# Kernel tuning notes

Hardware: AMD Instinct MI355X
Metric: run time of the kernel (lower is better)

Reference implementation:

```python
import jax, jax.numpy as jnp
import numpy as np
import math

N_ATOMS = 10000
N_EDGES = 100000
NF = 32          # num_radial_features
NK = 32          # radial basis size
CUTOFF = 5.0
L_BOND = 2       # max_basis_degree
L_IN = 2         # degree of atomic descriptors
L_OUT = 4        # max_degree of tensor product output
EPS = 1e-6

# ---------- real Clebsch-Gordan coefficients (built once in numpy) ----------

def _fact(n):
    return math.factorial(n)

def _cg_complex(j1, m1, j2, m2, j3, m3):
    if m1 + m2 != m3 or not (abs(j1 - j2) <= j3 <= j1 + j2):
        return 0.0
    if abs(m1) > j1 or abs(m2) > j2 or abs(m3) > j3:
        return 0.0
    pref = math.sqrt((2 * j3 + 1) * _fact(j3 + j1 - j2) * _fact(j3 - j1 + j2)
                     * _fact(j1 + j2 - j3) / _fact(j1 + j2 + j3 + 1))
    pref *= math.sqrt(_fact(j3 + m3) * _fact(j3 - m3) * _fact(j1 - m1)
                      * _fact(j1 + m1) * _fact(j2 - m2) * _fact(j2 + m2))
    s = 0.0
    for k in range(0, j1 + j2 - j3 + 1):
        d = [k, j1 + j2 - j3 - k, j1 - m1 - k, j2 + m2 - k, j3 - j2 + m1 + k, j3 - j1 - m2 + k]
        if min(d) < 0:
            continue
        s += (-1) ** k / float(_fact(d[0]) * _fact(d[1]) * _fact(d[2]) * _fact(d[3]) * _fact(d[4]) * _fact(d[5]))
    return pref * s

def _U(l):
    # unitary complex->real spherical harmonic change of basis, m ordered -l..l
    U = np.zeros((2 * l + 1, 2 * l + 1), dtype=complex)
    for m in range(-l, l + 1):
        i = m + l
        if m > 0:
            U[i, m + l] = (-1) ** m / math.sqrt(2.0)
            U[i, -m + l] = 1.0 / math.sqrt(2.0)
        elif m == 0:
            U[i, l] = 1.0
        else:
            U[i, m + l] = 1j / math.sqrt(2.0)
            U[i, -m + l] = -1j * (-1) ** (-m) / math.sqrt(2.0)
    return U

def _real_cg(l1, l2, l3):
    base = np.zeros((2 * l1 + 1, 2 * l2 + 1, 2 * l3 + 1))
    for m1 in range(-l1, l1 + 1):
        for m2 in range(-l2, l2 + 1):
            m3 = m1 + m2
            if abs(m3) <= l3:
                base[m1 + l1, m2 + l2, m3 + l3] = _cg_complex(l1, m1, l2, m2, l3, m3)
    C = np.einsum('ax,by,cz,xyz->abc', _U(l1).conj(), _U(l2).conj(), _U(l3), base)
    C = C.real if (l1 + l2 + l3) % 2 == 0 else C.imag  # odd paths -> pseudotensor channel
    return C.astype(np.float32)

def _build_paths():
    paths = []
    for l1 in range(L_BOND + 1):
        for l2 in range(L_IN + 1):
            for l3 in range(abs(l1 - l2), min(l1 + l2, L_OUT) + 1):
                par = (l1 + l2 + l3) % 2
                paths.append((l1, l2, l3, par, jnp.asarray(_real_cg(l1, l2, l3))))
    return paths

PATHS = _build_paths()
N_PATHS = len(PATHS)  # 19 paths

# ---------- equivariant building blocks ----------

def _dense(x, W, b):
    y = jnp.einsum('epmf,fg->epmg', x, W)
    return y.at[..., 0, :].add(b)

def _layernorm(x, gamma, beta):
    # equivariant LayerNorm: standard LN on scalars, per-degree RMS norm on l>0 blocks
    s = x[..., 0:1, :]
    mu = jnp.mean(s, axis=-1, keepdims=True)
    var = jnp.var(s, axis=-1, keepdims=True)
    parts = [(s - mu) / jnp.sqrt(var + EPS) * gamma[0] + beta]
    for l in range(1, L_IN + 1):
        blk = x[..., l * l:(l + 1) ** 2, :]
        rms = jnp.sqrt(jnp.mean(blk * blk, axis=(-2, -1), keepdims=True) + EPS)
        parts.append(blk / rms * gamma[l])
    return jnp.concatenate(parts, axis=-2)

def _mish_gate(x):
    s = x[..., 0:1, :]
    sp = jax.nn.softplus(s)
    t = jnp.tanh(sp)
    act = s * t
    d = t + s * (1.0 - t * t) * jax.nn.sigmoid(s)
    return jnp.concatenate([act, x[..., 1:, :] * d], axis=-2)

def _sph(u):
    # real spherical harmonics up to l=2, Racah normalization, m order -l..l
    x, y, z = u[:, 0], u[:, 1], u[:, 2]
    s3 = math.sqrt(3.0)
    return jnp.stack([jnp.ones_like(x), y, z, x,
                      s3 * x * y, s3 * y * z, 0.5 * (3.0 * z * z - 1.0),
                      s3 * x * z, 0.5 * s3 * (x * x - y * y)], axis=-1)  # (E, 9)

def _bond_basis(disp):
    r = jnp.sqrt(jnp.sum(disp * disp, axis=-1))          # (E,)
    u = disp / jnp.maximum(r, 1e-12)[:, None]
    centers = jnp.linspace(0.0, CUTOFF, NK)
    gamma = 0.5 * (NK / CUTOFF) ** 2
    rad = jnp.exp(-gamma * (r[:, None] - centers[None, :]) ** 2)  # (E, NK)
    cut = jnp.where(r < CUTOFF, 0.5 * (jnp.cos(jnp.pi * r / CUTOFF) + 1.0), 0.0)
    rad = rad * cut[:, None]
    sh = _sph(u)                                          # (E, 9)
    return sh[:, None, :, None] * rad[:, None, None, :]   # (E, 1, 9, NK)

def _tensor_product(x1, x2, tp_w):
    # CG-sparse equivariant tensor product with per-path per-feature weights
    E = x1.shape[0]
    F = x1.shape[-1]
    out = jnp.zeros((E, 2, (L_OUT + 1) ** 2, F), dtype=x1.dtype)
    for pidx, (l1, l2, l3, par, C) in enumerate(PATHS):
        a = x1[:, 0, l1 * l1:(l1 + 1) ** 2, :]
        b = x2[:, 0, l2 * l2:(l2 + 1) ** 2, :]
        seg = jnp.einsum('abc,eaf,ebf->ecf', C, a, b) * tp_w[pidx][None, None, :]
        out = out.at[:, par, l3 * l3:(l3 + 1) ** 2, :].add(seg)
    return out

# ---------- harness ----------

def setup_inputs() -> dict:
    key = jax.random.key(0)
    ks = jax.random.split(key, 8)
    atomic_descriptors = jax.random.normal(ks[0], (N_ATOMS, 1, (L_IN + 1) ** 2, NF), dtype=jnp.float32)
    neighbour_indices = jax.random.randint(ks[1], (N_EDGES, 2), 0, N_ATOMS, dtype=jnp.int32)
    neighbour_displacements = jax.random.normal(ks[2], (N_EDGES, 3), dtype=jnp.float32)
    W1 = jax.random.normal(ks[3], (NF, NF), dtype=jnp.float32) / math.sqrt(NF)
    b1 = jnp.zeros((NF,), dtype=jnp.float32)
    ln_gamma = jnp.ones((L_IN + 1, NF), dtype=jnp.float32)
    ln_beta = jnp.zeros((NF,), dtype=jnp.float32)
    W2 = jax.random.normal(ks[4], (NF, NF), dtype=jnp.float32) / math.sqrt(NF)
    b2 = jnp.zeros((NF,), dtype=jnp.float32)
    Wb = jax.random.normal(ks[5], (NK, NF), dtype=jnp.float32) / math.sqrt(NK)
    bb = jnp.zeros((NF,), dtype=jnp.float32)
    tp_w = jax.random.normal(ks[6], (N_PATHS, NF), dtype=jnp.float32) / math.sqrt(N_PATHS)
    return {"atomic_descriptors": atomic_descriptors,
            "neighbour_indices": neighbour_indices,
            "neighbour_displacements": neighbour_displacements,
            "W1": W1, "b1": b1, "ln_gamma": ln_gamma, "ln_beta": ln_beta,
            "W2": W2, "b2": b2, "Wb": Wb, "bb": bb, "tp_w": tp_w}

def reference(atomic_descriptors, neighbour_indices, neighbour_displacements,
              W1, b1, ln_gamma, ln_beta, W2, b2, Wb, bb, tp_w):
    i, j = neighbour_indices[:, 0], neighbour_indices[:, 1]
    y = atomic_descriptors[i] + atomic_descriptors[j]         # (E, 1, 9, F) gather + add
    y0 = _dense(y, W1, b1)
    y = _layernorm(y0, ln_gamma, ln_beta)
    y = _mish_gate(y)
    y = _dense(y, W2, b2) + y0                                # residual MLP
    basis = _bond_basis(neighbour_displacements)              # (E, 1, 9, NK)
    bexp = _dense(basis, Wb, bb)                              # (E, 1, 9, F)
    return _tensor_product(bexp, y, tp_w)                     # (E, 2, 25, F)
```

## Files before the change

kernel.cpp:

```cpp
#include <hip/hip_runtime.h>
#include <utility>

namespace cg {

constexpr double FACT[13] = {1.,1.,2.,6.,24.,120.,720.,5040.,40320.,362880.,
                             3628800.,39916800.,479001600.};

constexpr double csqrt(double x){
  if (x <= 0.0) return 0.0;
  double g = x > 1.0 ? x : 1.0;
  for (int i = 0; i < 80; i++) g = 0.5*(g + x/g);
  return g;
}

constexpr double cg_complex(int j1,int m1,int j2,int m2,int j3,int m3){
  if (m1+m2 != m3) return 0.0;
  int dj = j1>j2 ? j1-j2 : j2-j1;
  if (j3 < dj || j3 > j1+j2) return 0.0;
  int am1 = m1<0?-m1:m1, am2 = m2<0?-m2:m2, am3 = m3<0?-m3:m3;
  if (am1>j1 || am2>j2 || am3>j3) return 0.0;
  double pref = csqrt((2.0*j3+1.0)*FACT[j3+j1-j2]*FACT[j3-j1+j2]*FACT[j1+j2-j3]
                      /FACT[j1+j2+j3+1]);
  pref *= csqrt(FACT[j3+m3]*FACT[j3-m3]*FACT[j1-m1]*FACT[j1+m1]
               *FACT[j2-m2]*FACT[j2+m2]);
  double s = 0.0;
  for (int k = 0; k <= j1+j2-j3; k++){
    int d1=j1+j2-j3-k, d2=j1-m1-k, d3=j2+m2-k, d4=j3-j2+m1+k, d5=j3-j1-m2+k;
    if (d1<0||d2<0||d3<0||d4<0||d5<0) continue;
    double den = FACT[k]*FACT[d1]*FACT[d2]*FACT[d3]*FACT[d4]*FACT[d5];
    s += ((k&1) ? -1.0 : 1.0)/den;
  }
  return pref*s;
}

struct CD { double re, im; };
struct UMat { CD m[9][9]; };

constexpr UMat makeU(int l){
  UMat U{};
  const double is2 = 1.0/csqrt(2.0);
  for (int mm = -l; mm <= l; mm++){
    int i = mm + l;
    if (mm > 0){
      U.m[i][ mm+l] = CD{((mm&1)?-1.0:1.0)*is2, 0.0};
      U.m[i][-mm+l] = CD{is2, 0.0};
    } else if (mm == 0){
      U.m[i][l] = CD{1.0, 0.0};
    } else {
      int nm = -mm;
      U.m[i][mm+l] = CD{0.0, is2};
      U.m[i][nm+l] = CD{0.0, -((nm&1)?-1.0:1.0)*is2};
    }
  }
  return U;
}

struct CGT { double c[5][5][9]; };

constexpr CGT realCG(int l1,int l2,int l3){
  double base[5][5][9] = {};
  for (int m1 = -l1; m1 <= l1; m1++)
    for (int m2 = -l2; m2 <= l2; m2++){
      int m3 = m1 + m2;
      if (m3 >= -l3 && m3 <= l3)
        base[m1+l1][m2+l2][m3+l3] = cg_complex(l1,m1,l2,m2,l3,m3);
    }
  UMat U1 = makeU(l1), U2 = makeU(l2), U3 = makeU(l3);
  CGT R{};
  const int n1 = 2*l1+1, n2 = 2*l2+1, n3 = 2*l3+1;
  const bool even = ((l1+l2+l3)&1) == 0;
  for (int a = 0; a < n1; a++)
    for (int b = 0; b < n2; b++)
      for (int c = 0; c < n3; c++){
        double sre = 0.0, sim = 0.0;
        for (int x = 0; x < n1; x++){
          CD u1 = U1.m[a][x];
          if (u1.re == 0.0 && u1.im == 0.0) continue;
          u1.im = -u1.im;
          for (int y = 0; y < n2; y++){
            CD u2 = U2.m[b][y];
            if (u2.re == 0.0 && u2.im == 0.0) continue;
            u2.im = -u2.im;
            CD t12{u1.re*u2.re - u1.im*u2.im, u1.re*u2.im + u1.im*u2.re};
            for (int z = 0; z < n3; z++){
              double bs = base[x][y][z];
              if (bs == 0.0) continue;
              CD u3 = U3.m[c][z];
              if (u3.re == 0.0 && u3.im == 0.0) continue;
              sre += (t12.re*u3.re - t12.im*u3.im)*bs;
              sim += (t12.re*u3.im + t12.im*u3.re)*bs;
            }
          }
        }
        R.c[a][b][c] = even ? sre : sim;
      }
  return R;
}

constexpr int MAXE = 805;
struct Table {
  int n, np;
  int oc[MAXE]; int ia[MAXE]; int ib[MAXE]; int ip[MAXE];
  float v[MAXE];
};

constexpr Table buildTable(){
  Table t{};
  int n = 0, p = 0;
  for (int l1 = 0; l1 <= 2; l1++)
    for (int l2 = 0; l2 <= 2; l2++){
      int lo = l1 > l2 ? l1-l2 : l2-l1;
      int hi = (l1+l2) < 4 ? (l1+l2) : 4;
      for (int l3 = lo; l3 <= hi; l3++){
        int par = (l1+l2+l3)&1;
        CGT C = realCG(l1,l2,l3);
        for (int a = 0; a < 2*l1+1; a++)
          for (int b = 0; b < 2*l2+1; b++)
            for (int c = 0; c < 2*l3+1; c++){
              double v = C.c[a][b][c];
              if (v > 1e-10 || v < -1e-10){
                t.oc[n] = par*25 + l3*l3 + c;
                t.ia[n] = l1*l1 + a;
                t.ib[n] = l2*l2 + b;
                t.ip[n] = p;
                t.v[n]  = (float)v;
                n++;
              }
            }
        p++;
      }
    }
  t.n = n; t.np = p;
  return t;
}

constexpr Table T = buildTable();
static_assert(T.np == 19, "path count mismatch vs reference PATHS");
static_assert(T.n >= 19 && T.n <= MAXE, "nnz sanity");

}

template <int... Es>
__device__ __forceinline__ void tp_accum(float (&acc)[50], const float (&bx)[9],
                                         const float (&y2)[9], const float (&wv)[19],
                                         std::integer_sequence<int, Es...>){
  ( (acc[cg::T.oc[Es]] +=
       (cg::T.v[Es] * bx[cg::T.ia[Es]]) * (y2[cg::T.ib[Es]] * wv[cg::T.ip[Es]])), ... );
}

__global__ __launch_bounds__(256) void btmd_kernel(
    const float* __restrict__ A,  const int* __restrict__ NI,
    const float* __restrict__ D,
    const float* __restrict__ W1, const float* __restrict__ b1,
    const float* __restrict__ GM, const float* __restrict__ BT,
    const float* __restrict__ W2, const float* __restrict__ b2,
    const float* __restrict__ Wb, const float* __restrict__ bb,
    const float* __restrict__ TW, float* __restrict__ out, int nE)
{
  __shared__ alignas(16) float stg[8][288];
  __shared__ alignas(16) float radl[8][32];

  const int lane = threadIdx.x & 31;
  const int grp  = threadIdx.x >> 5;
  const int edge = blockIdx.x * 8 + grp;
  if (edge >= nE) return;

  const int ia_ = NI[2*edge + 0];
  const int ja_ = NI[2*edge + 1];
  const float* Ai = A + (size_t)ia_*288 + lane;
  const float* Aj = A + (size_t)ja_*288 + lane;
#pragma unroll
  for (int m = 0; m < 9; m++)
    stg[grp][m*32 + lane] = Ai[m*32] + Aj[m*32];

  const float dx = D[3*edge+0], dy = D[3*edge+1], dz = D[3*edge+2];
  const float r    = sqrtf(dx*dx + dy*dy + dz*dz);
  const float rinv = 1.0f / fmaxf(r, 1e-12f);
  const float ux = dx*rinv, uy = dy*rinv, uz = dz*rinv;
  const float S3 = 1.7320508075688772f;
  const float sh1 = uy, sh2 = uz, sh3 = ux;
  const float sh4 = S3*ux*uy, sh5 = S3*uy*uz;
  const float sh6 = 0.5f*(3.0f*uz*uz - 1.0f);
  const float sh7 = S3*ux*uz, sh8 = 0.5f*S3*(ux*ux - uy*uy);
  {
    const float ck  = (5.0f/31.0f)*(float)lane;
    const float dr  = r - ck;
    const float cut = (r < 5.0f)
        ? 0.5f*(__cosf(0.6283185307179586f*r) + 1.0f) : 0.0f;
    radl[grp][lane] = __expf(-20.48f*dr*dr) * cut;
  }

  float y0[9];
  {
    float w1c[32];
#pragma unroll
    for (int f = 0; f < 32; f++) w1c[f] = W1[f*32 + lane];
    const float b1v = b1[lane];
#pragma unroll
    for (int m = 0; m < 9; m++){
      float acc = (m == 0) ? b1v : 0.0f;
      const float4* s4 = (const float4*)(&stg[grp][m*32]);
#pragma unroll
      for (int q = 0; q < 8; q++){
        float4 a = s4[q];
        acc += a.x*w1c[4*q+0] + a.y*w1c[4*q+1] + a.z*w1c[4*q+2] + a.w*w1c[4*q+3];
      }
      y0[m] = acc;
    }
  }

  const float s0 = y0[0];
  float sum0 = s0, sumsq0 = s0*s0;
  float ss1 = y0[1]*y0[1] + y0[2]*y0[2] + y0[3]*y0[3];
  float ss2 = y0[4]*y0[4] + y0[5]*y0[5] + y0[6]*y0[6] + y0[7]*y0[7] + y0[8]*y0[8];
#pragma unroll
  for (int off = 16; off >= 1; off >>= 1){
    sum0   += __shfl_xor(sum0,   off, 32);
    sumsq0 += __shfl_xor(sumsq0, off, 32);
    ss1    += __shfl_xor(ss1,    off, 32);
    ss2    += __shfl_xor(ss2,    off, 32);
  }
  const float mu  = sum0*(1.0f/32.0f);
  const float var = sumsq0*(1.0f/32.0f) - mu*mu;
  const float g0 = GM[lane], g1 = GM[32+lane], g2 = GM[64+lane];
  const float shat = (s0 - mu)*rsqrtf(var + 1e-6f)*g0 + BT[lane];
  const float inv1 = rsqrtf(ss1*(1.0f/96.0f)  + 1e-6f)*g1;
  const float inv2 = rsqrtf(ss2*(1.0f/160.0f) + 1e-6f)*g2;

  const float s    = shat;
  const float sp   = fmaxf(s, 0.0f) + log1pf(__expf(-fabsf(s)));
  const float e2   = __expf(2.0f*sp);
  const float t    = 1.0f - 2.0f/(e2 + 1.0f);
  const float sig  = 1.0f/(1.0f + __expf(-s));
  const float dgat = t + s*(1.0f - t*t)*sig;
  const float act  = s*t;

  stg[grp][lane] = act;
#pragma unroll
  for (int m = 1; m < 4; m++) stg[grp][m*32 + lane] = y0[m]*inv1*dgat;
#pragma unroll
  for (int m = 4; m < 9; m++) stg[grp][m*32 + lane] = y0[m]*inv2*dgat;

  float y2[9];
  {
    float w2c[32];
#pragma unroll
    for (int f = 0; f < 32; f++) w2c[f] = W2[f*32 + lane];
    const float b2v = b2[lane];
#pragma unroll
    for (int m = 0; m < 9; m++){
      float acc = (m == 0) ? b2v : 0.0f;
      const float4* s4 = (const float4*)(&stg[grp][m*32]);
#pragma unroll
      for (int q = 0; q < 8; q++){
        float4 a = s4[q];
        acc += a.x*w2c[4*q+0] + a.y*w2c[4*q+1] + a.z*w2c[4*q+2] + a.w*w2c[4*q+3];
      }
      y2[m] = acc + y0[m];
    }
  }

  float gf;
  {
    float wbc[32];
#pragma unroll
    for (int k = 0; k < 32; k++) wbc[k] = Wb[k*32 + lane];
    float acc = 0.0f;
    const float4* r4 = (const float4*)(&radl[grp][0]);
#pragma unroll
    for (int q = 0; q < 8; q++){
      float4 a = r4[q];
      acc += a.x*wbc[4*q+0] + a.y*wbc[4*q+1] + a.z*wbc[4*q+2] + a.w*wbc[4*q+3];
    }
    gf = acc;
  }
  float bx[9];
  bx[0] = gf + bb[lane];
  bx[1] = sh1*gf; bx[2] = sh2*gf; bx[3] = sh3*gf; bx[4] = sh4*gf;
  bx[5] = sh5*gf; bx[6] = sh6*gf; bx[7] = sh7*gf; bx[8] = sh8*gf;

  float wv[19];
#pragma unroll
  for (int p = 0; p < 19; p++) wv[p] = TW[p*32 + lane];
  float acc[50];
#pragma unroll
  for (int c = 0; c < 50; c++) acc[c] = 0.0f;
  tp_accum(acc, bx, y2, wv, std::make_integer_sequence<int, cg::T.n>{});

  float* op = out + (size_t)edge*1600 + lane;
#pragma unroll
  for (int c = 0; c < 50; c++)
    __builtin_nontemporal_store(acc[c], op + c*32);
}

extern "C" void kernel_launch(void* const* d_in, const int* in_sizes, int n_in,
                              void* d_out, int out_size, void* d_ws, size_t ws_size,
                              hipStream_t stream)
{
  const float* A  = (const float*)d_in[0];
  const int*   NI = (const int*)  d_in[1];
  const float* D  = (const float*)d_in[2];
  const float* W1 = (const float*)d_in[3];
  const float* b1 = (const float*)d_in[4];
  const float* GM = (const float*)d_in[5];
  const float* BT = (const float*)d_in[6];
  const float* W2 = (const float*)d_in[7];
  const float* b2 = (const float*)d_in[8];
  const float* Wb = (const float*)d_in[9];
  const float* bb = (const float*)d_in[10];
  const float* TW = (const float*)d_in[11];
  float* out = (float*)d_out;

  const int nE = in_sizes[1] / 2;
  dim3 grid((nE + 7) / 8), block(256);
  btmd_kernel<<<grid, block, 0, stream>>>(A, NI, D, W1, b1, GM, BT, W2, b2,
                                          Wb, bb, TW, out, nE);
}
```

Measured before the change: 702.3 us.

## Persistent grid-stride kernel with prefetched gathers, LDS-staged weights, per-row TP stores

Converts the one-edge-per-warp launch into a persistent grid-stride kernel capped at 1024 blocks. Each block stages transposed W1/W2/Wb in shared memory once and keeps per-lane parameters in registers. The loop software-pipelines the next edge's descriptor gathers and the indices and displacements two edges ahead. The tensor product is reorganized by output channel so each output row is computed and stored immediately instead of holding 50 accumulators, aiming to cut register pressure (launch_bounds 256,4). The risk is extra registers from prefetch buffers and possible LDS bank conflicts on the transposed weight reads.

```diff
diff --git a/kernel.cpp b/kernel.cpp
--- a/kernel.cpp
+++ b/kernel.cpp
@@ -138,17 +138,54 @@
 static_assert(T.np == 19, "path count mismatch vs reference PATHS");
 static_assert(T.n >= 19 && T.n <= MAXE, "nnz sanity");
 
-}
-
-template <int... Es>
-__device__ __forceinline__ void tp_accum(float (&acc)[50], const float (&bx)[9],
-                                         const float (&y2)[9], const float (&wv)[19],
-                                         std::integer_sequence<int, Es...>){
-  ( (acc[cg::T.oc[Es]] +=
-       (cg::T.v[Es] * bx[cg::T.ia[Es]]) * (y2[cg::T.ib[Es]] * wv[cg::T.ip[Es]])), ... );
-}
-
-__global__ __launch_bounds__(256) void btmd_kernel(
+struct Table2 {
+  int off[51];
+  int ia[MAXE]; int ib[MAXE]; int ip[MAXE];
+  float v[MAXE];
+};
+
+constexpr Table2 buildTable2(){
+  Table2 s{};
+  int pos = 0;
+  for (int oc = 0; oc < 50; oc++){
+    s.off[oc] = pos;
+    for (int e = 0; e < T.n; e++){
+      if (T.oc[e] == oc){
+        s.ia[pos] = T.ia[e]; s.ib[pos] = T.ib[e];
+        s.ip[pos] = T.ip[e]; s.v[pos]  = T.v[e];
+        pos++;
+      }
+    }
+  }
+  s.off[50] = pos;
+  return s;
+}
+
+constexpr Table2 T2 = buildTable2();
+static_assert(T2.off[50] == T.n, "resort lost entries");
+
+}
+
+template <int OC, int B, int... Ks>
+__device__ __forceinline__ float tp_row(const float (&bx)[9], const float (&y2)[9],
+                                        const float (&wv)[19],
+                                        std::integer_sequence<int, Ks...>){
+  float a = 0.0f;
+  ((a += (cg::T2.v[B+Ks] * bx[cg::T2.ia[B+Ks]]) * (y2[cg::T2.ib[B+Ks]] * wv[cg::T2.ip[B+Ks]])), ...);
+  return a;
+}
+
+template <int... OCs>
+__device__ __forceinline__ void tp_store_all(const float (&bx)[9], const float (&y2)[9],
+                                             const float (&wv)[19], float* __restrict__ op,
+                                             std::integer_sequence<int, OCs...>){
+  ((__builtin_nontemporal_store(
+       tp_row<OCs, cg::T2.off[OCs]>(bx, y2, wv,
+         std::make_integer_sequence<int, cg::T2.off[OCs+1] - cg::T2.off[OCs]>{}),
+       op + OCs*32)), ...);
+}
+
+__global__ __launch_bounds__(256, 4) void btmd_kernel(
     const float* __restrict__ A,  const int* __restrict__ NI,
     const float* __restrict__ D,
     const float* __restrict__ W1, const float* __restrict__ b1,
@@ -159,138 +196,200 @@
 {
   __shared__ alignas(16) float stg[8][288];
   __shared__ alignas(16) float radl[8][32];
-
-  const int lane = threadIdx.x & 31;
-  const int grp  = threadIdx.x >> 5;
-  const int edge = blockIdx.x * 8 + grp;
-  if (edge >= nE) return;
-
-  const int ia_ = NI[2*edge + 0];
-  const int ja_ = NI[2*edge + 1];
-  const float* Ai = A + (size_t)ia_*288 + lane;
-  const float* Aj = A + (size_t)ja_*288 + lane;
-#pragma unroll
-  for (int m = 0; m < 9; m++)
-    stg[grp][m*32 + lane] = Ai[m*32] + Aj[m*32];
-
-  const float dx = D[3*edge+0], dy = D[3*edge+1], dz = D[3*edge+2];
-  const float r    = sqrtf(dx*dx + dy*dy + dz*dz);
-  const float rinv = 1.0f / fmaxf(r, 1e-12f);
-  const float ux = dx*rinv, uy = dy*rinv, uz = dz*rinv;
-  const float S3 = 1.7320508075688772f;
-  const float sh1 = uy, sh2 = uz, sh3 = ux;
-  const float sh4 = S3*ux*uy, sh5 = S3*uy*uz;
-  const float sh6 = 0.5f*(3.0f*uz*uz - 1.0f);
-  const float sh7 = S3*ux*uz, sh8 = 0.5f*S3*(ux*ux - uy*uy);
+  __shared__ alignas(16) float w1t[32*36];
+  __shared__ alignas(16) float w2t[32*36];
+  __shared__ alignas(16) float wbt[32*36];
+
+  const int tid  = threadIdx.x;
+  const int lane = tid & 31;
+  const int grp  = tid >> 5;
+
   {
-    const float ck  = (5.0f/31.0f)*(float)lane;
-    const float dr  = r - ck;
-    const float cut = (r < 5.0f)
-        ? 0.5f*(__cosf(0.6283185307179586f*r) + 1.0f) : 0.0f;
-    radl[grp][lane] = __expf(-20.48f*dr*dr) * cut;
-  }
-
-  float y0[9];
+    const int idx = tid*4;
+    const int f = idx >> 5, g = idx & 31;
+    const float4 a1 = *(const float4*)(W1 + idx);
+    const float4 a2 = *(const float4*)(W2 + idx);
+    const float4 a3 = *(const float4*)(Wb + idx);
+    w1t[(g+0)*36+f]=a1.x; w1t[(g+1)*36+f]=a1.y; w1t[(g+2)*36+f]=a1.z; w1t[(g+3)*36+f]=a1.w;
+    w2t[(g+0)*36+f]=a2.x; w2t[(g+1)*36+f]=a2.y; w2t[(g+2)*36+f]=a2.z; w2t[(g+3)*36+f]=a2.w;
+    wbt[(g+0)*36+f]=a3.x; wbt[(g+1)*36+f]=a3.y; wbt[(g+2)*36+f]=a3.z; wbt[(g+3)*36+f]=a3.w;
+  }
+
+  float wv[19];
+#pragma unroll
+  for (int p = 0; p < 19; p++) wv[p] = TW[p*32 + lane];
+  const float b1v = b1[lane], b2v = b2[lane], bbv = bb[lane];
+  const float g0 = GM[lane], g1 = GM[32+lane], g2 = GM[64+lane], btv = BT[lane];
+
+  __syncthreads();
+
+  const int stride = gridDim.x * 8;
+  int e = blockIdx.x * 8 + grp;
+  if (e >= nE) return;
+
+  float pa[9], pb[9];
+  float cdx, cdy, cdz;
+  int   i1 = 0, j1 = 0;
+  float d1x = 0.f, d1y = 0.f, d1z = 0.f;
+  int   i2 = 0, j2 = 0;
+  float d2x = 0.f, d2y = 0.f, d2z = 0.f;
+
   {
-    float w1c[32];
-#pragma unroll
-    for (int f = 0; f < 32; f++) w1c[f] = W1[f*32 + lane];
-    const float b1v = b1[lane];
-#pragma unroll
-    for (int m = 0; m < 9; m++){
-      float acc = (m == 0) ? b1v : 0.0f;
-      const float4* s4 = (const float4*)(&stg[grp][m*32]);
+    const int2 nn = *(const int2*)(NI + 2*e);
+    cdx = D[3*e]; cdy = D[3*e+1]; cdz = D[3*e+2];
+    const float* Ai = A + (size_t)nn.x*288 + lane;
+    const float* Aj = A + (size_t)nn.y*288 + lane;
+#pragma unroll
+    for (int m = 0; m < 9; m++){ pa[m] = Ai[m*32]; pb[m] = Aj[m*32]; }
+    const int en1 = e + stride;
+    if (en1 < nE){
+      const int2 n1 = *(const int2*)(NI + 2*en1);
+      i1 = n1.x; j1 = n1.y;
+      d1x = D[3*en1]; d1y = D[3*en1+1]; d1z = D[3*en1+2];
+    }
+  }
+
+  for (; e < nE; e += stride){
+    const int en1 = e + stride;
+    const int en2 = e + 2*stride;
+
+    if (en2 < nE){
+      const int2 n2 = *(const int2*)(NI + 2*en2);
+      i2 = n2.x; j2 = n2.y;
+      d2x = D[3*en2]; d2y = D[3*en2+1]; d2z = D[3*en2+2];
+    }
+
+#pragma unroll
+    for (int m = 0; m < 9; m++) stg[grp][m*32 + lane] = pa[m] + pb[m];
+
+    const float r    = sqrtf(cdx*cdx + cdy*cdy + cdz*cdz);
+    const float rinv = 1.0f / fmaxf(r, 1e-12f);
+    const float ux = cdx*rinv, uy = cdy*rinv, uz = cdz*rinv;
+    {
+      const float ck  = (5.0f/31.0f)*(float)lane;
+      const float dr  = r - ck;
+      const float cut = (r < 5.0f)
+          ? 0.5f*(__cosf(0.6283185307179586f*r) + 1.0f) : 0.0f;
+      radl[grp][lane] = __expf(-20.48f*dr*dr) * cut;
+    }
+
+    if (en1 < nE){
+      const float* Ai = A + (size_t)i1*288 + lane;
+      const float* Aj = A + (size_t)j1*288 + lane;
+#pragma unroll
+      for (int m = 0; m < 9; m++){ pa[m] = Ai[m*32]; pb[m] = Aj[m*32]; }
+    }
+
+    float y0[9];
+    {
+      float w1c[32];
+      const float4* wp = (const float4*)&w1t[lane*36];
 #pragma unroll
       for (int q = 0; q < 8; q++){
-        float4 a = s4[q];
-        acc += a.x*w1c[4*q+0] + a.y*w1c[4*q+1] + a.z*w1c[4*q+2] + a.w*w1c[4*q+3];
-      }
-      y0[m] = acc;
-    }
-  }
-
-  const float s0 = y0[0];
-  float sum0 = s0, sumsq0 = s0*s0;
-  float ss1 = y0[1]*y0[1] + y0[2]*y0[2] + y0[3]*y0[3];
-  float ss2 = y0[4]*y0[4] + y0[5]*y0[5] + y0[6]*y0[6] + y0[7]*y0[7] + y0[8]*y0[8];
-#pragma unroll
-  for (int off = 16; off >= 1; off >>= 1){
-    sum0   += __shfl_xor(sum0,   off, 32);
-    sumsq0 += __shfl_xor(sumsq0, off, 32);
-    ss1    += __shfl_xor(ss1,    off, 32);
-    ss2    += __shfl_xor(ss2,    off, 32);
-  }
-  const float mu  = sum0*(1.0f/32.0f);
-  const float var = sumsq0*(1.0f/32.0f) - mu*mu;
-  const float g0 = GM[lane], g1 = GM[32+lane], g2 = GM[64+lane];
-  const float shat = (s0 - mu)*rsqrtf(var + 1e-6f)*g0 + BT[lane];
-  const float inv1 = rsqrtf(ss1*(1.0f/96.0f)  + 1e-6f)*g1;
-  const float inv2 = rsqrtf(ss2*(1.0f/160.0f) + 1e-6f)*g2;
-
-  const float s    = shat;
-  const float sp   = fmaxf(s, 0.0f) + log1pf(__expf(-fabsf(s)));
-  const float e2   = __expf(2.0f*sp);
-  const float t    = 1.0f - 2.0f/(e2 + 1.0f);
-  const float sig  = 1.0f/(1.0f + __expf(-s));
-  const float dgat = t + s*(1.0f - t*t)*sig;
-  const float act  = s*t;
-
-  stg[grp][lane] = act;
-#pragma unroll
-  for (int m = 1; m < 4; m++) stg[grp][m*32 + lane] = y0[m]*inv1*dgat;
-#pragma unroll
-  for (int m = 4; m < 9; m++) stg[grp][m*32 + lane] = y0[m]*inv2*dgat;
-
-  float y2[9];
-  {
-    float w2c[32];
-#pragma unroll
-    for (int f = 0; f < 32; f++) w2c[f] = W2[f*32 + lane];
-    const float b2v = b2[lane];
-#pragma unroll
-    for (int m = 0; m < 9; m++){
-      float acc = (m == 0) ? b2v : 0.0f;
-      const float4* s4 = (const float4*)(&stg[grp][m*32]);
+        float4 w = wp[q];
+        w1c[4*q+0]=w.x; w1c[4*q+1]=w.y; w1c[4*q+2]=w.z; w1c[4*q+3]=w.w;
+      }
+#pragma unroll
+      for (int m = 0; m < 9; m++){
+        float acc = (m == 0) ? b1v : 0.0f;
+        const float4* s4 = (const float4*)(&stg[grp][m*32]);
+#pragma unroll
+        for (int q = 0; q < 8; q++){
+          float4 a = s4[q];
+          acc += a.x*w1c[4*q+0] + a.y*w1c[4*q+1] + a.z*w1c[4*q+2] + a.w*w1c[4*q+3];
+        }
+        y0[m] = acc;
+      }
+    }
+
+    const float s0 = y0[0];
+    float sum0 = s0, sumsq0 = s0*s0;
+    float ss1 = y0[1]*y0[1] + y0[2]*y0[2] + y0[3]*y0[3];
+    float ss2 = y0[4]*y0[4] + y0[5]*y0[5] + y0[6]*y0[6] + y0[7]*y0[7] + y0[8]*y0[8];
+#pragma unroll
+    for (int off = 16; off >= 1; off >>= 1){
+      sum0   += __shfl_xor(sum0,   off, 32);
+      sumsq0 += __shfl_xor(sumsq0, off, 32);
+      ss1    += __shfl_xor(ss1,    off, 32);
+      ss2    += __shfl_xor(ss2,    off, 32);
+    }
+    const float mu  = sum0*(1.0f/32.0f);
+    const float var = sumsq0*(1.0f/32.0f) - mu*mu;
+    const float shat = (s0 - mu)*rsqrtf(var + 1e-6f)*g0 + btv;
+    const float inv1 = rsqrtf(ss1*(1.0f/96.0f)  + 1e-6f)*g1;
+    const float inv2 = rsqrtf(ss2*(1.0f/160.0f) + 1e-6f)*g2;
+
+    const float s    = shat;
+    const float sp   = fmaxf(s, 0.0f) + log1pf(__expf(-fabsf(s)));
+    const float e2   = __expf(2.0f*sp);
+    const float t    = 1.0f - 2.0f/(e2 + 1.0f);
+    const float sig  = 1.0f/(1.0f + __expf(-s));
+    const float dgat = t + s*(1.0f - t*t)*sig;
+    const float act  = s*t;
+
+    stg[grp][lane] = act;
+#pragma unroll
+    for (int m = 1; m < 4; m++) stg[grp][m*32 + lane] = y0[m]*inv1*dgat;
+#pragma unroll
+    for (int m = 4; m < 9; m++) stg[grp][m*32 + lane] = y0[m]*inv2*dgat;
+
+    float y2[9];
+    {
+      float w2c[32];
+      const float4* wp = (const float4*)&w2t[lane*36];
 #pragma unroll
       for (int q = 0; q < 8; q++){
-        float4 a = s4[q];
-        acc += a.x*w2c[4*q+0] + a.y*w2c[4*q+1] + a.z*w2c[4*q+2] + a.w*w2c[4*q+3];
-      }
-      y2[m] = acc + y0[m];
-    }
-  }
-
-  float gf;
-  {
-    float wbc[32];
-#pragma unroll
-    for (int k = 0; k < 32; k++) wbc[k] = Wb[k*32 + lane];
-    float acc = 0.0f;
-    const float4* r4 = (const float4*)(&radl[grp][0]);
-#pragma unroll
-    for (int q = 0; q < 8; q++){
-      float4 a = r4[q];
-      acc += a.x*wbc[4*q+0] + a.y*wbc[4*q+1] + a.z*wbc[4*q+2] + a.w*wbc[4*q+3];
-    }
-    gf = acc;
-  }
-  float bx[9];
-  bx[0] = gf + bb[lane];
-  bx[1] = sh1*gf; bx[2] = sh2*gf; bx[3] = sh3*gf; bx[4] = sh4*gf;
-  bx[5] = sh5*gf; bx[6] = sh6*gf; bx[7] = sh7*gf; bx[8] = sh8*gf;
-
-  float wv[19];
-#pragma unroll
-  for (int p = 0; p < 19; p++) wv[p] = TW[p*32 + lane];
-  float acc[50];
-#pragma unroll
-  for (int c = 0; c < 50; c++) acc[c] = 0.0f;
-  tp_accum(acc, bx, y2, wv, std::make_integer_sequence<int, cg::T.n>{});
-
-  float* op = out + (size_t)edge*1600 + lane;
-#pragma unroll
-  for (int c = 0; c < 50; c++)
-    __builtin_nontemporal_store(acc[c], op + c*32);
+        float4 w = wp[q];
+        w2c[4*q+0]=w.x; w2c[4*q+1]=w.y; w2c[4*q+2]=w.z; w2c[4*q+3]=w.w;
+      }
+#pragma unroll
+      for (int m = 0; m < 9; m++){
+        float acc = (m == 0) ? b2v : 0.0f;
+        const float4* s4 = (const float4*)(&stg[grp][m*32]);
+#pragma unroll
+        for (int q = 0; q < 8; q++){
+          float4 a = s4[q];
+          acc += a.x*w2c[4*q+0] + a.y*w2c[4*q+1] + a.z*w2c[4*q+2] + a.w*w2c[4*q+3];
+        }
+        y2[m] = acc + y0[m];
+      }
+    }
+
+    float gf;
+    {
+      float wbc[32];
+      const float4* wp = (const float4*)&wbt[lane*36];
+#pragma unroll
+      for (int q = 0; q < 8; q++){
+        float4 w = wp[q];
+        wbc[4*q+0]=w.x; wbc[4*q+1]=w.y; wbc[4*q+2]=w.z; wbc[4*q+3]=w.w;
+      }
+      float acc = 0.0f;
+      const float4* r4 = (const float4*)(&radl[grp][0]);
+#pragma unroll
+      for (int q = 0; q < 8; q++){
+        float4 a = r4[q];
+        acc += a.x*wbc[4*q+0] + a.y*wbc[4*q+1] + a.z*wbc[4*q+2] + a.w*wbc[4*q+3];
+      }
+      gf = acc;
+    }
+
+    float bx[9];
+    {
+      const float S3 = 1.7320508075688772f;
+      bx[0] = gf + bbv;
+      bx[1] = uy*gf; bx[2] = uz*gf; bx[3] = ux*gf;
+      bx[4] = S3*ux*uy*gf; bx[5] = S3*uy*uz*gf;
+      bx[6] = 0.5f*(3.0f*uz*uz - 1.0f)*gf;
+      bx[7] = S3*ux*uz*gf; bx[8] = 0.5f*S3*(ux*ux - uy*uy)*gf;
+    }
+
+    float* op = out + (size_t)e*1600 + lane;
+    tp_store_all(bx, y2, wv, op, std::make_integer_sequence<int, 50>{});
+
+    cdx = d1x; cdy = d1y; cdz = d1z;
+    i1 = i2; j1 = j2; d1x = d2x; d1y = d2y; d1z = d2z;
+  }
 }
 
 extern "C" void kernel_launch(void* const* d_in, const int* in_sizes, int n_in,
@@ -312,7 +411,8 @@
   float* out = (float*)d_out;
 
   const int nE = in_sizes[1] / 2;
-  dim3 grid((nE + 7) / 8), block(256);
-  btmd_kernel<<<grid, block, 0, stream>>>(A, NI, D, W1, b1, GM, BT, W2, b2,
-                                          Wb, bb, TW, out, nE);
-}
+  int grid = (nE + 7) / 8;
+  if (grid > 1024) grid = 1024;
+  btmd_kernel<<<dim3(grid), dim3(256), 0, stream>>>(A, NI, D, W1, b1, GM, BT,
+                                                    W2, b2, Wb, bb, TW, out, nE);
+}
```

New measurement: 1.462 ms. 108% more time.
